# Kernel tuning notes

Measured on AMD Instinct MI355X. Metric: run time of the kernel, lower is better.

Reference implementation:

```python
import jax, jax.numpy as jnp
import numpy as np
from jax import lax

L = 4096          # sequence length (timesteps)
N_ITEMS = 512     # number of items == RNN input_size (x[:,:,k] is (L, N))
HIDDEN = 256
NUM_LAYERS = 16
NUM_FEATURES = 4
OUT_SIZE = 2


def _rnn_params(key, input_size):
    """Vanilla tanh RNN params, PyTorch-style uniform(-1/sqrt(H), 1/sqrt(H))."""
    ks = jax.random.split(key, 5)
    s = 1.0 / np.sqrt(HIDDEN)
    u = lambda k, shape: jax.random.uniform(k, shape, jnp.float32, -s, s)
    return dict(
        Wih0=u(ks[0], (HIDDEN, input_size)),              # layer 0 input weights
        Wih=u(ks[1], (NUM_LAYERS - 1, HIDDEN, HIDDEN)),   # layers 1..15 input weights
        Whh=u(ks[2], (NUM_LAYERS, HIDDEN, HIDDEN)),
        bih=u(ks[3], (NUM_LAYERS, HIDDEN)),
        bhh=u(ks[4], (NUM_LAYERS, HIDDEN)),
    )


def setup_inputs() -> dict:
    key = jax.random.key(0)
    kx, k1, k2, k3 = jax.random.split(key, 4)
    x = jax.random.normal(kx, (L, N_ITEMS, NUM_FEATURES), jnp.float32)
    lp = _rnn_params(k1, N_ITEMS)    # self.low_price (used for features 0, 2, 3)
    lpv = _rnn_params(k2, N_ITEMS)   # self.low_price_vol (used for feature 1)
    kf1, kf2 = jax.random.split(k3)
    s = 1.0 / np.sqrt(HIDDEN * NUM_FEATURES)
    fc_W = jax.random.uniform(kf1, (OUT_SIZE, HIDDEN * NUM_FEATURES), jnp.float32, -s, s)
    fc_b = jax.random.uniform(kf2, (OUT_SIZE,), jnp.float32, -s, s)
    return {
        "x": x,
        "lp_Wih0": lp["Wih0"], "lp_Wih": lp["Wih"], "lp_Whh": lp["Whh"],
        "lp_bih": lp["bih"], "lp_bhh": lp["bhh"],
        "lpv_Wih0": lpv["Wih0"], "lpv_Wih": lpv["Wih"], "lpv_Whh": lpv["Whh"],
        "lpv_bih": lpv["bih"], "lpv_bhh": lpv["bhh"],
        "fc_W": fc_W, "fc_b": fc_b,
    }


def _run_rnn(seq, Wih0, Wih, Whh, bih, bhh):
    """Multi-layer vanilla tanh RNN over an unbatched (L, input_size) sequence.
    Returns the top-layer hidden state at the last timestep, shape (HIDDEN,)."""

    def step(h, x_t):  # h: (NUM_LAYERS, HIDDEN); x_t: (input_size,)
        inp = jnp.tanh(Wih0 @ x_t + bih[0] + Whh[0] @ h[0] + bhh[0])
        hs = [inp]
        for l in range(1, NUM_LAYERS):
            inp = jnp.tanh(Wih[l - 1] @ inp + bih[l] + Whh[l] @ h[l] + bhh[l])
            hs.append(inp)
        return jnp.stack(hs), None

    h0 = jnp.zeros((NUM_LAYERS, HIDDEN), seq.dtype)
    h_final, _ = lax.scan(step, h0, seq)
    return h_final[-1]


def reference(x, lp_Wih0, lp_Wih, lp_Whh, lp_bih, lp_bhh,
              lpv_Wih0, lpv_Wih, lpv_Whh, lpv_bih, lpv_bhh, fc_W, fc_b):
    lp = (lp_Wih0, lp_Wih, lp_Whh, lp_bih, lp_bhh)
    lpv = (lpv_Wih0, lpv_Wih, lpv_Whh, lpv_bih, lpv_bhh)
    # Faithful to the original (buggy) forward: low_price for features 0,2,3;
    # low_price_vol for feature 1.
    h0 = _run_rnn(x[:, :, 0], *lp)
    h1 = _run_rnn(x[:, :, 1], *lpv)
    h2 = _run_rnn(x[:, :, 2], *lp)
    h3 = _run_rnn(x[:, :, 3], *lp)
    out = jnp.concatenate([h0, h1, h2, h3])  # (4*HIDDEN,)
    return fc_W @ out + fc_b  # (OUT_SIZE,)
```

## Files before the change

kernel.cpp:

```cpp
#include <hip/hip_runtime.h>
#include <hip/hip_bf16.h>
#include <math.h>

#define SEQL   4096
#define NITEMS 512
#define HID    256
#define NLAY   16
#define QS     64
#define CHUNK  8
#define NCHUNK (SEQL / CHUNK)
#define TPB    4

typedef float f4 __attribute__((ext_vector_type(4)));

#define P_OFF   ((size_t)0)
#define H_OFF   (P_OFF + (size_t)4*SEQL*HID)
#define AP_OFF  (H_OFF + (size_t)4*NLAY*QS*HID)
#define HF_OFF  (AP_OFF + (size_t)4*NLAY*QS*HID)
#define FLAG_OFF_FLOATS (HF_OFF + (size_t)1024)
#define NFLAGS 256

__device__ __forceinline__ float ld_coh_b32(const float* p) {
    float r;
    asm volatile("global_load_dword %0, %1, off sc0 sc1" : "=v"(r) : "v"(p));
    return r;
}
__device__ __forceinline__ void st_coh_b32(float* p, float v) {
    asm volatile("global_store_dword %0, %1, off sc0 sc1" :: "v"(p), "v"(v) : "memory");
}
__device__ __forceinline__ void st_coh_u32(unsigned* p, unsigned v) {
    asm volatile("global_store_dword %0, %1, off sc0 sc1" :: "v"(p), "v"(v) : "memory");
}
__device__ __forceinline__ unsigned uload(const unsigned* p) {
    return __hip_atomic_load(p, __ATOMIC_RELAXED, __HIP_MEMORY_SCOPE_AGENT);
}

#define SBAR()  { __builtin_amdgcn_s_barrier(); __builtin_amdgcn_sched_barrier(0); }
#define LGKM0() { asm volatile("s_waitcnt lgkmcnt(0)" ::: "memory"); __builtin_amdgcn_sched_barrier(0); }
#define VMW0()  { asm volatile("s_waitcnt vmcnt(0)" ::: "memory"); __builtin_amdgcn_sched_barrier(0); }

__device__ __forceinline__ void spin_ge(const unsigned* p, unsigned target, bool* dead) {
    if (*dead) return;
    unsigned it = 0;
    while (uload(p) < target) {
        __builtin_amdgcn_s_sleep(1);
        if (++it > (1u << 20)) { *dead = true; break; }
    }
}

__device__ __forceinline__ float tanh_fast(float x) {
    return 1.f - __fdividef(2.f, __expf(2.f * x) + 1.f);
}

#define FMAC0(ACC, HB, W) \
    asm volatile("v_fmac_f32 %0, %1, %2" : "+v"(ACC) : "v"(HB), "v"(W));
#define FMACR(ACC, HB, W, I) \
    asm volatile("v_fmac_f32_dpp %0, %1, %2 row_ror:" #I " row_mask:0xf bank_mask:0xf" \
                 : "+v"(ACC) : "v"(HB), "v"(W));

#define FMAC_BLOCK(HB, WB) \
    FMAC0(acc0, HB, w[WB+0])      FMACR(acc1, HB, w[WB+1], 1)   \
    FMACR(acc2, HB, w[WB+2], 2)   FMACR(acc3, HB, w[WB+3], 3)   \
    FMACR(acc0, HB, w[WB+4], 4)   FMACR(acc1, HB, w[WB+5], 5)   \
    FMACR(acc2, HB, w[WB+6], 6)   FMACR(acc3, HB, w[WB+7], 7)   \
    FMACR(acc0, HB, w[WB+8], 8)   FMACR(acc1, HB, w[WB+9], 9)   \
    FMACR(acc2, HB, w[WB+10], 10) FMACR(acc3, HB, w[WB+11], 11) \
    FMACR(acc0, HB, w[WB+12], 12) FMACR(acc1, HB, w[WB+13], 13) \
    FMACR(acc2, HB, w[WB+14], 14) FMACR(acc3, HB, w[WB+15], 15)

#define BPERM4(H) \
    { hb0 = __int_as_float(__builtin_amdgcn_ds_bpermute(ab0, __float_as_int(H))); \
      hb1 = __int_as_float(__builtin_amdgcn_ds_bpermute(ab1, __float_as_int(H))); \
      hb2 = __int_as_float(__builtin_amdgcn_ds_bpermute(ab2, __float_as_int(H))); \
      hb3 = __int_as_float(__builtin_amdgcn_ds_bpermute(ab3, __float_as_int(H))); }

__global__ __launch_bounds__(1024) void proj_kernel(
    const float* __restrict__ x, const float* __restrict__ Wlp,
    const float* __restrict__ Wlpv, float* __restrict__ P)
{
    __shared__ float xs[TPB][4][NITEMS];
    const int tid = threadIdx.x;
    const int t0 = blockIdx.x * TPB;

    #pragma unroll
    for (int tt = 0; tt < TPB; ++tt) {
        const float2* src = (const float2*)(x + (size_t)(t0 + tt) * NITEMS * 4);
        float2 v = src[tid];
        int e = 2 * tid;
        xs[tt][e & 3][e >> 2]       = v.x;
        xs[tt][(e + 1) & 3][e >> 2] = v.y;
    }
    __syncthreads();

    const int c = tid >> 8, j = tid & 255;
    const float* W = (c == 1) ? Wlpv : Wlp;
    const float4* row = (const float4*)(W + (size_t)j * NITEMS);
    float acc[TPB] = {0.f, 0.f, 0.f, 0.f};
    #pragma unroll 4
    for (int k4 = 0; k4 < NITEMS / 4; ++k4) {
        float4 w = row[k4];
        #pragma unroll
        for (int tt = 0; tt < TPB; ++tt) {
            float4 xv = *(const float4*)(&xs[tt][c][k4 * 4]);
            acc[tt] = fmaf(w.x, xv.x, fmaf(w.y, xv.y, fmaf(w.z, xv.z, fmaf(w.w, xv.w, acc[tt]))));
        }
    }
    #pragma unroll
    for (int tt = 0; tt < TPB; ++tt)
        P[((size_t)c * SEQL + (t0 + tt)) * HID + j] = acc[tt];
}

__global__ __launch_bounds__(1024) void rnn_pipe(
    const float* __restrict__ lp_Wih,  const float* __restrict__ lp_Whh,
    const float* __restrict__ lp_bih,  const float* __restrict__ lp_bhh,
    const float* __restrict__ lpv_Wih, const float* __restrict__ lpv_Whh,
    const float* __restrict__ lpv_bih, const float* __restrict__ lpv_bhh,
    const float* __restrict__ P, float* __restrict__ Hring,
    float* __restrict__ Apart, float* __restrict__ hfinal,
    unsigned* __restrict__ Hflag, unsigned* __restrict__ Aflag)
{
    __shared__ __align__(16) float part2[2][1024];

    const int b = blockIdx.x;
    if (b >= 124) return;
    const int tid = threadIdx.x;

    const int c = b / 31;
    const int r = b % 31;
    const int role = (r < NLAY) ? 0 : 1;
    const int l = (r < NLAY) ? r : (r - NLAY + 1);

    const float* Wih = (c == 1) ? lpv_Wih : lp_Wih;
    const float* Whh = (c == 1) ? lpv_Whh : lp_Whh;
    const float* bih = (c == 1) ? lpv_bih : lp_bih;
    const float* bhh = (c == 1) ? lpv_bhh : lp_bhh;

    const int j    = tid & 255;
    const int c4   = tid >> 8;
    const int lane = tid & 63;
    const int q    = lane & 15;
    const int m    = (c4 << 6) | lane;
    const bool first = ((tid & 192) == 0);
    bool dead = false;

    const int ab0 = 4 * (q);
    const int ab1 = 4 * (16 + q);
    const int ab2 = 4 * (32 + q);
    const int ab3 = 4 * (48 + q);

    if (role == 0) {
        const bool l0 = (l == 0);

        float w[64];
        {
            const float* Wrow = Whh + ((size_t)l * HID + j) * HID;
            #pragma unroll
            for (int bb = 0; bb < 4; ++bb)
                #pragma unroll
                for (int i = 0; i < 16; ++i)
                    w[bb * 16 + i] = Wrow[(c4 << 6) + bb * 16 + ((q - i) & 15)];
        }
        #pragma unroll
        for (int i = 0; i < 64; ++i) asm volatile("" : "+v"(w[i]));

        const float bias_m = bih[l * HID + m] + bhh[l * HID + m];

        const float*    Psrc  = P + (size_t)c * SEQL * HID;
        const float*    apbuf = Apart + ((size_t)(c * NLAY + l) * QS) * HID;
        const unsigned* af    = Aflag + c * NLAY + l;
        unsigned*       myHfl = Hflag + c * NLAY + l;
        const unsigned* consA = Aflag + c * NLAY + l + 1;
        float*          Hout  = Hring + ((size_t)(c * NLAY + l) * QS) * HID;
        float*          hfin  = hfinal + (size_t)c * HID;

        float h = 0.f;
        float hb0, hb1, hb2, hb3;

        for (int k = 0; k < NCHUNK; ++k) {
            if (tid == 0) {
                if (!l0) spin_ge(af, (unsigned)(k + 1), &dead);
                if (l < NLAY - 1 && k >= CHUNK) spin_ge(consA, (unsigned)(k - 7), &dead);
            }
            SBAR();
            float ap8[CHUNK];
            if (l0) {
                #pragma unroll
                for (int s = 0; s < CHUNK; ++s)
                    ap8[s] = Psrc[(size_t)(CHUNK * k + s) * HID + m];
            } else {
                const int sbase = (k & 7) * CHUNK;
                #pragma unroll
                for (int s = 0; s < CHUNK; ++s)
                    ap8[s] = ld_coh_b32(apbuf + (size_t)(sbase + s) * HID + m);
                VMW0();
            }
            #pragma unroll
            for (int s = 0; s < CHUNK; ++s) {
                BPERM4(h);
                float acc0 = 0.f, acc1 = 0.f, acc2 = 0.f, acc3 = 0.f;
                FMAC_BLOCK(hb0, 0)
                FMAC_BLOCK(hb1, 16)
                FMAC_BLOCK(hb2, 32)
                FMAC_BLOCK(hb3, 48)
                part2[s & 1][tid] = (acc0 + acc1) + (acc2 + acc3);
                LGKM0(); SBAR();
                const float* pb = &part2[s & 1][0];
                float p = pb[m] + pb[m + 256] + pb[m + 512] + pb[m + 768];
                h = tanh_fast(p + ap8[s] + bias_m);
                if (first) {
                    if (l < NLAY - 1)
                        st_coh_b32(Hout + (size_t)((k & 7) * CHUNK + s) * HID + m, h);
                    else if (k == NCHUNK - 1 && s == CHUNK - 1)
                        st_coh_b32(hfin + m, h);
                }
            }
            if (first) VMW0();
            SBAR();
            if (tid == 0) st_coh_u32(myHfl, (unsigned)(k + 1));
        }
    } else {
        float w[64];
        {
            const float* Wrow = Wih + ((size_t)(l - 1) * HID + j) * HID;
            #pragma unroll
            for (int bb = 0; bb < 4; ++bb)
                #pragma unroll
                for (int i = 0; i < 16; ++i)
                    w[bb * 16 + i] = Wrow[(c4 << 6) + bb * 16 + ((q - i) & 15)];
        }
        #pragma unroll
        for (int i = 0; i < 64; ++i) asm volatile("" : "+v"(w[i]));

        const float*    Hin    = Hring + ((size_t)(c * NLAY + (l - 1)) * QS) * HID;
        const unsigned* inflag = Hflag + c * NLAY + (l - 1);
        float*          Aout   = Apart + ((size_t)(c * NLAY + l) * QS) * HID;
        unsigned*       myAfl  = Aflag + c * NLAY + l;
        const unsigned* consB  = Hflag + c * NLAY + l;

        float hb0, hb1, hb2, hb3;

        for (int k = 0; k < NCHUNK; ++k) {
            if (tid == 0) {
                spin_ge(inflag, (unsigned)(k + 1), &dead);
                if (k >= CHUNK) spin_ge(consB, (unsigned)(k - 7), &dead);
            }
            SBAR();
            float h8[CHUNK];
            {
                const float* hbase = Hin + (size_t)(k & 7) * CHUNK * HID + m;
                #pragma unroll
                for (int s = 0; s < CHUNK; ++s)
                    h8[s] = ld_coh_b32(hbase + (size_t)s * HID);
                VMW0();
            }
            #pragma unroll
            for (int s = 0; s < CHUNK; ++s) {
                BPERM4(h8[s]);
                float acc0 = 0.f, acc1 = 0.f, acc2 = 0.f, acc3 = 0.f;
                FMAC_BLOCK(hb0, 0)
                FMAC_BLOCK(hb1, 16)
                FMAC_BLOCK(hb2, 32)
                FMAC_BLOCK(hb3, 48)
                part2[s & 1][tid] = (acc0 + acc1) + (acc2 + acc3);
                LGKM0(); SBAR();
                if (first) {
                    const float* pb = &part2[s & 1][0];
                    float p = pb[m] + pb[m + 256] + pb[m + 512] + pb[m + 768];
                    st_coh_b32(Aout + (size_t)((k & 7) * CHUNK + s) * HID + m, p);
                }
            }
            if (first) VMW0();
            SBAR();
            if (tid == 0) st_coh_u32(myAfl, (unsigned)(k + 1));
        }
    }
}

__global__ __launch_bounds__(1024) void fc_kernel(
    const float* __restrict__ hfinal, const float* __restrict__ fcW,
    const float* __restrict__ fcb, float* __restrict__ out)
{
    __shared__ float red[1024];
    const int tid = threadIdx.x;
    float v  = hfinal[tid];
    float p0 = fcW[tid] * v;
    float p1 = fcW[1024 + tid] * v;

    red[tid] = p0; __syncthreads();
    for (int st = 512; st > 0; st >>= 1) { if (tid < st) red[tid] += red[tid + st]; __syncthreads(); }
    if (tid == 0) out[0] = red[0] + fcb[0];
    __syncthreads();
    red[tid] = p1; __syncthreads();
    for (int st = 512; st > 0; st >>= 1) { if (tid < st) red[tid] += red[tid + st]; __syncthreads(); }
    if (tid == 0) out[1] = red[0] + fcb[1];
}

extern "C" void kernel_launch(void* const* d_in, const int* in_sizes, int n_in,
                              void* d_out, int out_size, void* d_ws, size_t ws_size,
                              hipStream_t stream)
{
    (void)in_sizes; (void)n_in; (void)out_size; (void)ws_size;
    const float* x        = (const float*)d_in[0];
    const float* lp_Wih0  = (const float*)d_in[1];
    const float* lp_Wih   = (const float*)d_in[2];
    const float* lp_Whh   = (const float*)d_in[3];
    const float* lp_bih   = (const float*)d_in[4];
    const float* lp_bhh   = (const float*)d_in[5];
    const float* lpv_Wih0 = (const float*)d_in[6];
    const float* lpv_Wih  = (const float*)d_in[7];
    const float* lpv_Whh  = (const float*)d_in[8];
    const float* lpv_bih  = (const float*)d_in[9];
    const float* lpv_bhh  = (const float*)d_in[10];
    const float* fcW      = (const float*)d_in[11];
    const float* fcb      = (const float*)d_in[12];

    float* ws      = (float*)d_ws;
    float* Pbuf    = ws + P_OFF;
    float* Hring   = ws + H_OFF;
    float* Apart   = ws + AP_OFF;
    float* hfinal  = ws + HF_OFF;
    unsigned* flags = (unsigned*)(ws + FLAG_OFF_FLOATS);

    hipMemsetAsync(flags, 0, NFLAGS * sizeof(unsigned), stream);

    proj_kernel<<<SEQL / TPB, 1024, 0, stream>>>(x, lp_Wih0, lpv_Wih0, Pbuf);

    rnn_pipe<<<124, 1024, 0, stream>>>(lp_Wih, lp_Whh, lp_bih, lp_bhh,
                                       lpv_Wih, lpv_Whh, lpv_bih, lpv_bhh,
                                       Pbuf, Hring, Apart, hfinal,
                                       flags, flags + 64);

    fc_kernel<<<1, 1024, 0, stream>>>(hfinal, fcW, fcb, (float*)d_out);
}
```

Baseline: 4.286 ms.

## Prefetch next chunk inputs and poll pipeline flags during compute

Both RNN roles now issue asynchronous flag polls (on threads 64/65) at the start of each chunk and check them mid-chunk. If the producer is already ahead, they prefetch the next chunk's activations into registers while the current chunk computes. At the next chunk boundary this lets the block skip the tid-0 spin-wait and block barrier, so the serial handoff latency between pipeline stages leaves the critical path. The accumulator assignment inside the DPP FMA block is also reshuffled. The cost is more registers, extra LDS flag traffic, and conservative fallbacks when polled flags are stale.

Result: faster. 3.806 ms (median of 2 runs) (-11.2%).

```diff
diff --git a/kernel.cpp b/kernel.cpp
--- a/kernel.cpp
+++ b/kernel.cpp
@@ -38,6 +38,8 @@
 #define SBAR()  { __builtin_amdgcn_s_barrier(); __builtin_amdgcn_sched_barrier(0); }
 #define LGKM0() { asm volatile("s_waitcnt lgkmcnt(0)" ::: "memory"); __builtin_amdgcn_sched_barrier(0); }
 #define VMW0()  { asm volatile("s_waitcnt vmcnt(0)" ::: "memory"); __builtin_amdgcn_sched_barrier(0); }
+#define WAIT_PIN(reg) { asm volatile("s_waitcnt vmcnt(0)" : "+v"(reg) :: "memory"); \
+                        __builtin_amdgcn_sched_barrier(0); }
 
 __device__ __forceinline__ void spin_ge(const unsigned* p, unsigned target, bool* dead) {
     if (*dead) return;
@@ -64,8 +66,8 @@
     FMACR(acc0, HB, w[WB+4], 4)   FMACR(acc1, HB, w[WB+5], 5)   \
     FMACR(acc2, HB, w[WB+6], 6)   FMACR(acc3, HB, w[WB+7], 7)   \
     FMACR(acc0, HB, w[WB+8], 8)   FMACR(acc1, HB, w[WB+9], 9)   \
-    FMACR(acc2, HB, w[WB+10], 10) FMACR(acc3, HB, w[WB+11], 11) \
-    FMACR(acc0, HB, w[WB+12], 12) FMACR(acc1, HB, w[WB+13], 13) \
+    FMACR(acc0, HB, w[WB+10], 10) FMACR(acc1, HB, w[WB+11], 11) \
+    FMACR(acc2, HB, w[WB+12], 12) FMACR(acc3, HB, w[WB+13], 13) \
     FMACR(acc2, HB, w[WB+14], 14) FMACR(acc3, HB, w[WB+15], 15)
 
 #define BPERM4(H) \
@@ -120,6 +122,7 @@
     unsigned* __restrict__ Hflag, unsigned* __restrict__ Aflag)
 {
     __shared__ __align__(16) float part2[2][1024];
+    __shared__ int pf_lds[2];
 
     const int b = blockIdx.x;
     if (b >= 124) return;
@@ -175,25 +178,45 @@
 
         float h = 0.f;
         float hb0, hb1, hb2, hb3;
+        float ap8[CHUNK], apn[CHUNK];
+        bool havePF = false;
 
         for (int k = 0; k < NCHUNK; ++k) {
-            if (tid == 0) {
-                if (!l0) spin_ge(af, (unsigned)(k + 1), &dead);
-                if (l < NLAY - 1 && k >= CHUNK) spin_ge(consA, (unsigned)(k - 7), &dead);
-            }
-            SBAR();
-            float ap8[CHUNK];
-            if (l0) {
+            int pf2ok = 1;
+            if (k >= CHUNK && l < NLAY - 1) pf2ok = pf_lds[1];
+            const bool needbar = (!havePF && !l0) || !pf2ok;
+            if (needbar) {
+                if (tid == 0) {
+                    if (!havePF && !l0) spin_ge(af, (unsigned)(k + 1), &dead);
+                    if (!pf2ok) spin_ge(consA, (unsigned)(k - 7), &dead);
+                }
+                SBAR();
+            }
+            if (havePF) {
+                VMW0();
                 #pragma unroll
-                for (int s = 0; s < CHUNK; ++s)
-                    ap8[s] = Psrc[(size_t)(CHUNK * k + s) * HID + m];
+                for (int s = 0; s < CHUNK; ++s) ap8[s] = apn[s];
             } else {
-                const int sbase = (k & 7) * CHUNK;
-                #pragma unroll
-                for (int s = 0; s < CHUNK; ++s)
-                    ap8[s] = ld_coh_b32(apbuf + (size_t)(sbase + s) * HID + m);
-                VMW0();
-            }
+                if (l0) {
+                    #pragma unroll
+                    for (int s = 0; s < CHUNK; ++s)
+                        ap8[s] = Psrc[(size_t)(CHUNK * k + s) * HID + m];
+                } else {
+                    const int sbase = (k & 7) * CHUNK;
+                    #pragma unroll
+                    for (int s = 0; s < CHUNK; ++s)
+                        ap8[s] = ld_coh_b32(apbuf + (size_t)(sbase + s) * HID + m);
+                    VMW0();
+                }
+            }
+            unsigned afv = 0u, bpv = 0u;
+            const bool pollIn = (!l0) && (k + 1 < NCHUNK);
+            const bool pollBp = (l < NLAY - 1) && (k + 1 >= CHUNK) && (k + 1 < NCHUNK);
+            if (tid == 64 && pollIn)
+                asm volatile("global_load_dword %0, %1, off sc0 sc1" : "=v"(afv) : "v"(af));
+            if (tid == 65 && pollBp)
+                asm volatile("global_load_dword %0, %1, off sc0 sc1" : "=v"(bpv) : "v"(consA));
+
             #pragma unroll
             for (int s = 0; s < CHUNK; ++s) {
                 BPERM4(h);
@@ -213,6 +236,29 @@
                     else if (k == NCHUNK - 1 && s == CHUNK - 1)
                         st_coh_b32(hfin + m, h);
                 }
+                if (s == 1) {
+                    if (tid == 64 && pollIn) { WAIT_PIN(afv); pf_lds[0] = (afv >= (unsigned)(k + 2)); }
+                    if (tid == 65 && pollBp) { WAIT_PIN(bpv); pf_lds[1] = (bpv >= (unsigned)(k - 6)); }
+                }
+                if (s == 2) {
+                    havePF = false;
+                    if (k + 1 < NCHUNK) {
+                        const bool b1 = l0 || (pf_lds[0] != 0);
+                        if (b1) {
+                            havePF = true;
+                            if (l0) {
+                                #pragma unroll
+                                for (int s2 = 0; s2 < CHUNK; ++s2)
+                                    apn[s2] = Psrc[(size_t)(CHUNK * (k + 1) + s2) * HID + m];
+                            } else {
+                                const int nb = ((k + 1) & 7) * CHUNK;
+                                #pragma unroll
+                                for (int s2 = 0; s2 < CHUNK; ++s2)
+                                    apn[s2] = ld_coh_b32(apbuf + (size_t)(nb + s2) * HID + m);
+                            }
+                        }
+                    }
+                }
             }
             if (first) VMW0();
             SBAR();
@@ -238,21 +284,39 @@
         const unsigned* consB  = Hflag + c * NLAY + l;
 
         float hb0, hb1, hb2, hb3;
+        float h8[CHUNK], h8n[CHUNK];
+        bool havePF = false;
 
         for (int k = 0; k < NCHUNK; ++k) {
-            if (tid == 0) {
-                spin_ge(inflag, (unsigned)(k + 1), &dead);
-                if (k >= CHUNK) spin_ge(consB, (unsigned)(k - 7), &dead);
-            }
-            SBAR();
-            float h8[CHUNK];
-            {
+            int pf2ok = 1;
+            if (k >= CHUNK) pf2ok = pf_lds[1];
+            const bool needbar = !havePF || !pf2ok;
+            if (needbar) {
+                if (tid == 0) {
+                    if (!havePF) spin_ge(inflag, (unsigned)(k + 1), &dead);
+                    if (!pf2ok)  spin_ge(consB, (unsigned)(k - 7), &dead);
+                }
+                SBAR();
+            }
+            if (havePF) {
+                VMW0();
+                #pragma unroll
+                for (int s = 0; s < CHUNK; ++s) h8[s] = h8n[s];
+            } else {
                 const float* hbase = Hin + (size_t)(k & 7) * CHUNK * HID + m;
                 #pragma unroll
                 for (int s = 0; s < CHUNK; ++s)
                     h8[s] = ld_coh_b32(hbase + (size_t)s * HID);
                 VMW0();
             }
+            unsigned inv = 0u, bpv = 0u;
+            const bool pollIn = (k + 1 < NCHUNK);
+            const bool pollBp = (k + 1 >= CHUNK) && (k + 1 < NCHUNK);
+            if (tid == 64 && pollIn)
+                asm volatile("global_load_dword %0, %1, off sc0 sc1" : "=v"(inv) : "v"(inflag));
+            if (tid == 65 && pollBp)
+                asm volatile("global_load_dword %0, %1, off sc0 sc1" : "=v"(bpv) : "v"(consB));
+
             #pragma unroll
             for (int s = 0; s < CHUNK; ++s) {
                 BPERM4(h8[s]);
@@ -267,6 +331,20 @@
                     const float* pb = &part2[s & 1][0];
                     float p = pb[m] + pb[m + 256] + pb[m + 512] + pb[m + 768];
                     st_coh_b32(Aout + (size_t)((k & 7) * CHUNK + s) * HID + m, p);
+                }
+                if (s == 1) {
+                    if (tid == 64 && pollIn) { WAIT_PIN(inv); pf_lds[0] = (inv >= (unsigned)(k + 2)); }
+                    if (tid == 65 && pollBp) { WAIT_PIN(bpv); pf_lds[1] = (bpv >= (unsigned)(k - 6)); }
+                }
+                if (s == 2) {
+                    havePF = false;
+                    if (k + 1 < NCHUNK && pf_lds[0] != 0) {
+                        havePF = true;
+                        const float* nb = Hin + (size_t)((k + 1) & 7) * CHUNK * HID + m;
+                        #pragma unroll
+                        for (int s2 = 0; s2 < CHUNK; ++s2)
+                            h8n[s2] = ld_coh_b32(nb + (size_t)s2 * HID);
+                    }
                 }
             }
             if (first) VMW0();
```
